# Kernel tuning notes

Measured on AMD Instinct MI355X. Metric: run time of the kernel, lower is better.

## Reference

```python
import jax, jax.numpy as jnp
import numpy as np

D_MODEL = 1024
D_HIDDEN = 4096
NUM_EXPERTS = 8
K_ACTIVE = 2


def setup_inputs() -> dict:
    key = jax.random.key(0)
    ks = jax.random.split(key, 8)
    x = jax.random.normal(ks[0], (1, 2048, D_MODEL), dtype=jnp.float32)
    gate_w = jax.random.normal(ks[1], (D_MODEL, NUM_EXPERTS), dtype=jnp.float32) * 0.02
    gate_b = jnp.zeros((NUM_EXPERTS,), dtype=jnp.float32)
    w1 = jax.random.normal(ks[2], (NUM_EXPERTS, D_MODEL, D_HIDDEN), dtype=jnp.float32) * 0.02
    b1 = jnp.zeros((NUM_EXPERTS, D_HIDDEN), dtype=jnp.float32)
    w2 = jax.random.normal(ks[3], (NUM_EXPERTS, D_HIDDEN, D_MODEL), dtype=jnp.float32) * 0.02
    b2 = jnp.zeros((NUM_EXPERTS, D_MODEL), dtype=jnp.float32)
    return {"x": x, "gate_w": gate_w, "gate_b": gate_b,
            "w1": w1, "b1": b1, "w2": w2, "b2": b2}


def reference(x, gate_w, gate_b, w1, b1, w2, b2):
    B, S, D = x.shape
    xf = x.reshape(-1, D)                                    # [T, D]
    logits = xf @ gate_w + gate_b                            # [T, E]
    top_w, top_idx = jax.lax.top_k(logits, K_ACTIVE)         # [T, K]
    top_w = jax.nn.softmax(top_w, axis=-1)                   # softmax over selected experts
    # combine-weight per expert: sum over k slots of one-hot(idx) * weight -> [T, E]
    gates = jnp.sum(jax.nn.one_hot(top_idx, NUM_EXPERTS, dtype=xf.dtype) * top_w[..., None], axis=1)
    # expert FFN applied per expert (dropout is identity in eval): gelu is exact (erf), matching torch nn.GELU default
    h = jax.nn.gelu(jnp.einsum('td,edh->teh', xf, w1) + b1[None], approximate=False)  # [T, E, H]
    y = jnp.einsum('teh,ehd->ted', h, w2) + b2[None]         # [T, E, D]
    out = jnp.einsum('ted,te->td', y, gates)                 # weighted combine of selected experts
    return out.reshape(B, S, D)
```

## Files before the change

kernel.cpp:

```cpp
#include <hip/hip_runtime.h>
#include <stdint.h>

typedef unsigned short u16;
typedef __attribute__((ext_vector_type(8))) short s16x8;
typedef __attribute__((ext_vector_type(8))) u16  u16x8;
typedef __attribute__((ext_vector_type(4))) u16  u16x4;
typedef __attribute__((ext_vector_type(4))) float f32x4;

#define T_TOKENS 2048
#define DM 1024
#define DH 4096
#define NE 8
#define BM 128
#define BN 128
#define BN2 64
#define BK 64
#define MAXSLOTS (T_TOKENS*2 + NE*BM)
#define ROWBLK (MAXSLOTS/BM)

__device__ __forceinline__ u16 f2bf(float f) {
    union { float ff; uint32_t u; } v; v.ff = f;
    uint32_t r = v.u + 0x7fffu + ((v.u >> 16) & 1u);
    return (u16)(r >> 16);
}

#define GLOAD_LDS16(gsrc, ldst) \
    __builtin_amdgcn_global_load_lds((const __attribute__((address_space(1))) uint32_t*)(gsrc), \
                                     (__attribute__((address_space(3))) uint32_t*)(ldst), 16, 0, 0)

__global__ void k_convert(const float* __restrict__ x, u16* __restrict__ xbf,
                          int* __restrict__ ctrl) {
    int i = blockIdx.x * blockDim.x + threadIdx.x;
    const f32x4* xv = (const f32x4*)x;
    f32x4 a = xv[2*i], b = xv[2*i+1];
    u16x8 o;
    o[0]=f2bf(a[0]); o[1]=f2bf(a[1]); o[2]=f2bf(a[2]); o[3]=f2bf(a[3]);
    o[4]=f2bf(b[0]); o[5]=f2bf(b[1]); o[6]=f2bf(b[2]); o[7]=f2bf(b[3]);
    ((u16x8*)xbf)[i] = o;
    if (blockIdx.x == 0 && threadIdx.x < 32) ctrl[threadIdx.x] = 0;
}

__global__ void __launch_bounds__(256) k_transpose(const float* __restrict__ src,
                                                   u16* __restrict__ dst,
                                                   int K, int N) {
    __shared__ float tile[64][65];
    const int e = blockIdx.z;
    const int n0 = blockIdx.x * 64, k0 = blockIdx.y * 64;
    const float* s = src + (size_t)e * K * N;
    u16* d = dst + (size_t)e * K * N;
    const int tx = threadIdx.x & 15, ty = threadIdx.x >> 4;
    #pragma unroll
    for (int j = 0; j < 4; ++j) {
        int r = ty * 4 + j;
        f32x4 v = *(const f32x4*)(s + (size_t)(k0 + r) * N + n0 + tx * 4);
        tile[r][tx*4+0] = v[0]; tile[r][tx*4+1] = v[1];
        tile[r][tx*4+2] = v[2]; tile[r][tx*4+3] = v[3];
    }
    __syncthreads();
    #pragma unroll
    for (int j = 0; j < 4; ++j) {
        int n = ty * 4 + j;
        u16x4 w;
        #pragma unroll
        for (int c = 0; c < 4; ++c) w[c] = f2bf(tile[tx*4+c][n]);
        *(u16x4*)(d + (size_t)(n0 + n) * K + k0 + tx * 4) = w;
    }
}

__global__ void __launch_bounds__(64) k_gate(const float* __restrict__ x,
                                             const float* __restrict__ gw,
                                             const float* __restrict__ gb,
                                             int* __restrict__ cnt,
                                             int* __restrict__ tt_idx,
                                             float* __restrict__ tt_w) {
    const int t = blockIdx.x;
    const int lane = threadIdx.x;
    float acc[NE] = {0.f,0.f,0.f,0.f,0.f,0.f,0.f,0.f};
    const float* xr = x + (size_t)t * DM;
    #pragma unroll
    for (int c = 0; c < DM/64; ++c) {
        float xv = xr[lane + 64*c];
        const float* g = gw + (size_t)(lane + 64*c) * NE;
        #pragma unroll
        for (int e = 0; e < NE; ++e) acc[e] += xv * g[e];
    }
    #pragma unroll
    for (int e = 0; e < NE; ++e) {
        #pragma unroll
        for (int off = 32; off >= 1; off >>= 1)
            acc[e] += __shfl_xor(acc[e], off, 64);
    }
    if (lane == 0) {
        float l[NE];
        #pragma unroll
        for (int e = 0; e < NE; ++e) l[e] = acc[e] + gb[e];
        int i0 = 0;
        #pragma unroll
        for (int e = 1; e < NE; ++e) if (l[e] > l[i0]) i0 = e;
        int i1 = (i0 == 0) ? 1 : 0;
        #pragma unroll
        for (int e = 0; e < NE; ++e) if (e != i0 && l[e] > l[i1]) i1 = e;
        float m  = l[i0];
        float w0 = expf(l[i0] - m), w1 = expf(l[i1] - m);
        float s = w0 + w1; w0 /= s; w1 /= s;
        tt_idx[t*2] = i0; tt_idx[t*2+1] = i1;
        tt_w[t*2] = w0;  tt_w[t*2+1] = w1;
        atomicAdd(&cnt[i0], 1); atomicAdd(&cnt[i1], 1);
    }
}

__global__ void k_offsets(const int* __restrict__ cnt, int* __restrict__ fill,
                          int* __restrict__ off) {
    if (threadIdx.x == 0 && blockIdx.x == 0) {
        int a = 0;
        for (int e = 0; e < NE; ++e) {
            off[e] = a;
            a += (cnt[e] + BM - 1) / BM * BM;
            fill[e] = 0;
        }
        off[NE] = a;
    }
}

__global__ void k_scatter(const int* __restrict__ tt_idx, const float* __restrict__ tt_w,
                          const int* __restrict__ off, int* __restrict__ fill,
                          int* __restrict__ slot_token, float* __restrict__ slot_gate) {
    int t = blockIdx.x * blockDim.x + threadIdx.x;
    if (t >= T_TOKENS) return;
    #pragma unroll
    for (int k = 0; k < 2; ++k) {
        int e = tt_idx[t*2+k];
        int pos = off[e] + atomicAdd(&fill[e], 1);
        slot_token[pos] = t;
        slot_gate[pos]  = tt_w[t*2+k];
    }
}

__device__ __forceinline__ void mma64(const u16* As, const u16* Bs, int lane,
                                      int wr, int wc, f32x4 acc[4][4]) {
    #pragma unroll
    for (int ko = 0; ko < 2; ++ko) {
        s16x8 af[4], bfr[4];
        #pragma unroll
        for (int m = 0; m < 4; ++m) {
            int row = wr*64 + m*16 + (lane & 15);
            int sl = (ko*4 + (lane >> 4)) ^ (row & 7);
            af[m] = *(const s16x8*)&As[row*BK + sl*8];
        }
        #pragma unroll
        for (int n = 0; n < 4; ++n) {
            int col = wc*64 + n*16 + (lane & 15);
            int sl = (ko*4 + (lane >> 4)) ^ (col & 7);
            bfr[n] = *(const s16x8*)&Bs[col*BK + sl*8];
        }
        #pragma unroll
        for (int m = 0; m < 4; ++m)
            #pragma unroll
            for (int n = 0; n < 4; ++n)
                acc[m][n] = __builtin_amdgcn_mfma_f32_16x16x32_bf16(af[m], bfr[n], acc[m][n], 0, 0, 0);
    }
}

__device__ __forceinline__ void mma64_n2(const u16* As, const u16* Bs, int lane,
                                         int wr, int wc, f32x4 acc[4][2]) {
    #pragma unroll
    for (int ko = 0; ko < 2; ++ko) {
        s16x8 af[4], bfr[2];
        #pragma unroll
        for (int m = 0; m < 4; ++m) {
            int row = wr*64 + m*16 + (lane & 15);
            int sl = (ko*4 + (lane >> 4)) ^ (row & 7);
            af[m] = *(const s16x8*)&As[row*BK + sl*8];
        }
        #pragma unroll
        for (int n = 0; n < 2; ++n) {
            int col = wc*32 + n*16 + (lane & 15);
            int sl = (ko*4 + (lane >> 4)) ^ (col & 7);
            bfr[n] = *(const s16x8*)&Bs[col*BK + sl*8];
        }
        #pragma unroll
        for (int m = 0; m < 4; ++m)
            #pragma unroll
            for (int n = 0; n < 2; ++n)
                acc[m][n] = __builtin_amdgcn_mfma_f32_16x16x32_bf16(af[m], bfr[n], acc[m][n], 0, 0, 0);
    }
}


__global__ void __launch_bounds__(256) k_ffn1_b16(
    const u16* __restrict__ xbf, const u16* __restrict__ w1t,
    const float* __restrict__ b1, const int* __restrict__ slot_token,
    const int* __restrict__ off, u16* __restrict__ h)
{
    __shared__ u16 As[2][BM*BK];
    __shared__ u16 Bs[2][BN*BK];
    const int rb = blockIdx.y, cb = blockIdx.x;
    const int total = off[NE];
    const int r0 = rb * BM;
    if (r0 >= total) return;
    int e = 0;
    while (e < NE-1 && off[e+1] <= r0) e++;
    const u16* Bsrc = w1t + (size_t)e * DM * DH;
    const float* be = b1 + (size_t)e * DH;

    const int tid = threadIdx.x;
    const int lane = tid & 63, wid = tid >> 6;
    const int wr = wid >> 1, wc = wid & 1;

    const u16* gA[4]; const u16* gB[4];
    #pragma unroll
    for (int i = 0; i < 4; ++i) {
        int row = wid*32 + i*8 + (lane >> 3);
        int g = (lane & 7) ^ (row & 7);
        int tok = slot_token[r0 + row];
        gA[i] = xbf + (size_t)tok * DM + g*8;
        gB[i] = Bsrc + (size_t)(cb*BN + row) * DM + g*8;
    }

    f32x4 acc[4][4];
    #pragma unroll
    for (int m = 0; m < 4; ++m)
        #pragma unroll
        for (int n = 0; n < 4; ++n) acc[m][n] = (f32x4){0.f,0.f,0.f,0.f};

    #define STAGE1(buf, kt) do {                                              \
        _Pragma("unroll")                                                     \
        for (int i = 0; i < 4; ++i) {                                         \
            GLOAD_LDS16(gA[i] + (kt)*BK, &As[buf][(wid*32 + i*8)*BK]);        \
            GLOAD_LDS16(gB[i] + (kt)*BK, &Bs[buf][(wid*32 + i*8)*BK]);        \
        }                                                                     \
    } while (0)

    const int NT = DM / BK;
    STAGE1(0, 0);
    __syncthreads();
    #pragma unroll 1
    for (int kt = 0; kt < NT; kt += 2) {
        STAGE1(1, kt + 1);
        mma64(As[0], Bs[0], lane, wr, wc, acc);
        __syncthreads();
        if (kt + 2 < NT) STAGE1(0, kt + 2);
        mma64(As[1], Bs[1], lane, wr, wc, acc);
        __syncthreads();
    }
    #undef STAGE1

    #pragma unroll
    for (int n = 0; n < 4; ++n) {
        int col = cb*BN + wc*64 + n*16 + (lane & 15);
        float bb = be[col];
        #pragma unroll
        for (int m = 0; m < 4; ++m) {
            int rbase = r0 + wr*64 + m*16 + (lane >> 4)*4;
            #pragma unroll
            for (int i = 0; i < 4; ++i) {
                float v = acc[m][n][i] + bb;
                float gv = 0.5f * v * (1.0f + erff(v * 0.70710678118654752f));
                h[(size_t)(rbase + i)*DH + col] = f2bf(gv);
            }
        }
    }
}

__global__ void __launch_bounds__(256) k_ffn2_b16(
    const u16* __restrict__ h, const u16* __restrict__ w2t,
    const float* __restrict__ b2, const int* __restrict__ slot_token,
    const float* __restrict__ slot_gate, const int* __restrict__ off,
    float* __restrict__ out)
{
    __shared__ u16 As[2][BM*BK];
    __shared__ u16 Bs[2][BN2*BK];
    const int rb = blockIdx.y, cb = blockIdx.x;
    const int total = off[NE];
    const int r0 = rb * BM;
    if (r0 >= total) return;
    int e = 0;
    while (e < NE-1 && off[e+1] <= r0) e++;
    const u16* Bsrc = w2t + (size_t)e * DH * DM;
    const float* be = b2 + (size_t)e * DM;

    const int tid = threadIdx.x;
    const int lane = tid & 63, wid = tid >> 6;
    const int wr = wid >> 1, wc = wid & 1;

    const u16* gA[4]; const u16* gB[2];
    #pragma unroll
    for (int i = 0; i < 4; ++i) {
        int row = wid*32 + i*8 + (lane >> 3);
        int g = (lane & 7) ^ (row & 7);
        gA[i] = h + (size_t)(r0 + row) * DH + g*8;
    }
    #pragma unroll
    for (int i = 0; i < 2; ++i) {
        int n = wid*16 + i*8 + (lane >> 3);
        int g = (lane & 7) ^ (n & 7);
        gB[i] = Bsrc + (size_t)(cb*BN2 + n) * DH + g*8;
    }

    f32x4 acc[4][2];
    #pragma unroll
    for (int m = 0; m < 4; ++m)
        #pragma unroll
        for (int n = 0; n < 2; ++n) acc[m][n] = (f32x4){0.f,0.f,0.f,0.f};

    #define STAGE2(buf, kt) do {                                              \
        _Pragma("unroll")                                                     \
        for (int i = 0; i < 4; ++i)                                           \
            GLOAD_LDS16(gA[i] + (kt)*BK, &As[buf][(wid*32 + i*8)*BK]);        \
        _Pragma("unroll")                                                     \
        for (int i = 0; i < 2; ++i)                                           \
            GLOAD_LDS16(gB[i] + (kt)*BK, &Bs[buf][(wid*16 + i*8)*BK]);        \
    } while (0)

    const int NT = DH / BK;
    STAGE2(0, 0);
    __syncthreads();
    #pragma unroll 1
    for (int kt = 0; kt < NT; kt += 2) {
        STAGE2(1, kt + 1);
        mma64_n2(As[0], Bs[0], lane, wr, wc, acc);
        __syncthreads();
        if (kt + 2 < NT) STAGE2(0, kt + 2);
        mma64_n2(As[1], Bs[1], lane, wr, wc, acc);
        __syncthreads();
    }
    #undef STAGE2

    float bb[2];
    #pragma unroll
    for (int n = 0; n < 2; ++n) bb[n] = be[cb*BN2 + wc*32 + n*16 + (lane & 15)];
    #pragma unroll
    for (int m = 0; m < 4; ++m) {
        #pragma unroll
        for (int i = 0; i < 4; ++i) {
            int s = r0 + wr*64 + m*16 + (lane >> 4)*4 + i;
            int tok = slot_token[s];
            float g = slot_gate[s];
            if (g != 0.0f) {
                float* orow = out + (size_t)tok * DM + cb*BN2 + wc*32;
                #pragma unroll
                for (int n = 0; n < 2; ++n)
                    atomicAdd(orow + n*16 + (lane & 15), g * (acc[m][n][i] + bb[n]));
            }
        }
    }
}


__global__ void __launch_bounds__(256) k_ffn1_f32(
    const u16* __restrict__ xbf, const float* __restrict__ w1,
    const float* __restrict__ b1, const int* __restrict__ slot_token,
    const int* __restrict__ off, u16* __restrict__ h)
{
    __shared__ u16 As[BM*BK];
    __shared__ u16 Bs[BN*BK];
    const int rb = blockIdx.y, cb = blockIdx.x;
    const int total = off[NE];
    const int r0 = rb * BM;
    if (r0 >= total) return;
    int e = 0;
    while (e < NE-1 && off[e+1] <= r0) e++;
    const float* Bsrc = w1 + (size_t)e * DM * DH;
    const float* be   = b1 + (size_t)e * DH;

    const int tid = threadIdx.x;
    const int lane = tid & 63, wid = tid >> 6;
    const int wr = wid >> 1, wc = wid & 1;

    const u16* gA[4];
    #pragma unroll
    for (int i = 0; i < 4; ++i) {
        int row = wid*32 + i*8 + (lane >> 3);
        int g = (lane & 7) ^ (row & 7);
        int tok = slot_token[r0 + row];
        gA[i] = xbf + (size_t)tok * DM + g*8;
    }
    const int tc = tid & 31, tr = tid >> 5;
    const float* gB = Bsrc + (size_t)(tr*8) * DH + cb*BN + tc*4;

    f32x4 acc[4][4];
    #pragma unroll
    for (int m = 0; m < 4; ++m)
        #pragma unroll
        for (int n = 0; n < 4; ++n) acc[m][n] = (f32x4){0.f,0.f,0.f,0.f};

    for (int kt = 0; kt < DM/BK; ++kt) {
        #pragma unroll
        for (int i = 0; i < 4; ++i)
            GLOAD_LDS16(gA[i] + kt*BK, &As[(wid*32 + i*8)*BK]);
        f32x4 bv[8];
        #pragma unroll
        for (int j = 0; j < 8; ++j)
            bv[j] = *(const f32x4*)(gB + (size_t)(kt*BK + j) * DH);
        #pragma unroll
        for (int c = 0; c < 4; ++c) {
            int n = tc*4 + c;
            int sl = tr ^ (n & 7);
            s16x8 pk;
            #pragma unroll
            for (int j = 0; j < 8; ++j) pk[j] = (short)f2bf(bv[j][c]);
            *(s16x8*)&Bs[n*BK + sl*8] = pk;
        }
        __syncthreads();
        mma64(As, Bs, lane, wr, wc, acc);
        __syncthreads();
    }
    #pragma unroll
    for (int n = 0; n < 4; ++n) {
        int col = cb*BN + wc*64 + n*16 + (lane & 15);
        float bb = be[col];
        #pragma unroll
        for (int m = 0; m < 4; ++m) {
            int rbase = r0 + wr*64 + m*16 + (lane >> 4)*4;
            #pragma unroll
            for (int i = 0; i < 4; ++i) {
                float v = acc[m][n][i] + bb;
                float gv = 0.5f * v * (1.0f + erff(v * 0.70710678118654752f));
                h[(size_t)(rbase + i)*DH + col] = f2bf(gv);
            }
        }
    }
}

__global__ void __launch_bounds__(256) k_ffn2_f32(
    const u16* __restrict__ h, const float* __restrict__ w2,
    const float* __restrict__ b2, const int* __restrict__ slot_token,
    const float* __restrict__ slot_gate, const int* __restrict__ off,
    float* __restrict__ out)
{
    __shared__ u16 As[BM*BK];
    __shared__ u16 Bs[BN*BK];
    const int rb = blockIdx.y, cb = blockIdx.x;
    const int total = off[NE];
    const int r0 = rb * BM;
    if (r0 >= total) return;
    int e = 0;
    while (e < NE-1 && off[e+1] <= r0) e++;
    const float* Bsrc = w2 + (size_t)e * DH * DM;
    const float* be   = b2 + (size_t)e * DM;

    const int tid = threadIdx.x;
    const int lane = tid & 63, wid = tid >> 6;
    const int wr = wid >> 1, wc = wid & 1;

    const u16* gA[4];
    #pragma unroll
    for (int i = 0; i < 4; ++i) {
        int row = wid*32 + i*8 + (lane >> 3);
        int g = (lane & 7) ^ (row & 7);
        gA[i] = h + (size_t)(r0 + row) * DH + g*8;
    }
    const int tc = tid & 31, tr = tid >> 5;
    const float* gB = Bsrc + (size_t)(tr*8) * DM + cb*BN + tc*4;

    f32x4 acc[4][4];
    #pragma unroll
    for (int m = 0; m < 4; ++m)
        #pragma unroll
        for (int n = 0; n < 4; ++n) acc[m][n] = (f32x4){0.f,0.f,0.f,0.f};

    for (int kt = 0; kt < DH/BK; ++kt) {
        #pragma unroll
        for (int i = 0; i < 4; ++i)
            GLOAD_LDS16(gA[i] + kt*BK, &As[(wid*32 + i*8)*BK]);
        f32x4 bv[8];
        #pragma unroll
        for (int j = 0; j < 8; ++j)
            bv[j] = *(const f32x4*)(gB + (size_t)(kt*BK + j) * DM);
        #pragma unroll
        for (int c = 0; c < 4; ++c) {
            int n = tc*4 + c;
            int sl = tr ^ (n & 7);
            s16x8 pk;
            #pragma unroll
            for (int j = 0; j < 8; ++j) pk[j] = (short)f2bf(bv[j][c]);
            *(s16x8*)&Bs[n*BK + sl*8] = pk;
        }
        __syncthreads();
        mma64(As, Bs, lane, wr, wc, acc);
        __syncthreads();
    }
    float bb[4];
    #pragma unroll
    for (int n = 0; n < 4; ++n) bb[n] = be[cb*BN + wc*64 + n*16 + (lane & 15)];
    #pragma unroll
    for (int m = 0; m < 4; ++m) {
        #pragma unroll
        for (int i = 0; i < 4; ++i) {
            int s = r0 + wr*64 + m*16 + (lane >> 4)*4 + i;
            int tok = slot_token[s];
            float g = slot_gate[s];
            if (g != 0.0f) {
                float* orow = out + (size_t)tok * DM + cb*BN + wc*64;
                #pragma unroll
                for (int n = 0; n < 4; ++n)
                    atomicAdd(orow + n*16 + (lane & 15), g * (acc[m][n][i] + bb[n]));
            }
        }
    }
}

extern "C" void kernel_launch(void* const* d_in, const int* in_sizes, int n_in,
                              void* d_out, int out_size, void* d_ws, size_t ws_size,
                              hipStream_t stream)
{
    (void)in_sizes; (void)n_in; (void)out_size;
    const float* x  = (const float*)d_in[0];
    const float* gw = (const float*)d_in[1];
    const float* gb = (const float*)d_in[2];
    const float* w1 = (const float*)d_in[3];
    const float* b1 = (const float*)d_in[4];
    const float* w2 = (const float*)d_in[5];
    const float* b2 = (const float*)d_in[6];
    float* out = (float*)d_out;
    char* ws = (char*)d_ws;

    const size_t OFF_XBF = 0;
    const size_t OFF_H   = 4194304;
    const size_t OFF_WT  = OFF_H + (size_t)MAXSLOTS * DH * 2;
    const size_t OFF_ST  = OFF_WT + (size_t)NE * DM * DH * 2;
    const size_t OFF_SG  = OFF_ST + MAXSLOTS * 4;
    const size_t OFF_TI  = OFF_SG + MAXSLOTS * 4;
    const size_t OFF_TW  = OFF_TI + T_TOKENS * 2 * 4;
    const size_t OFF_CT  = OFF_TW + T_TOKENS * 2 * 4;
    const size_t NEED_B16 = OFF_CT + 128;

    if (ws_size >= NEED_B16) {
        u16*   xbf        = (u16*)(ws + OFF_XBF);
        u16*   h          = (u16*)(ws + OFF_H);
        u16*   wt         = (u16*)(ws + OFF_WT);
        int*   slot_token = (int*)(ws + OFF_ST);
        float* slot_gate  = (float*)(ws + OFF_SG);
        int*   tt_idx     = (int*)(ws + OFF_TI);
        float* tt_w       = (float*)(ws + OFF_TW);
        int*   ctrl       = (int*)(ws + OFF_CT);
        int* cnt = ctrl; int* fill = ctrl + 8; int* offs = ctrl + 16;

        hipMemsetAsync(slot_token, 0, 2 * MAXSLOTS * 4, stream);
        hipMemsetAsync(out, 0, (size_t)T_TOKENS * DM * sizeof(float), stream);

        k_convert<<<(T_TOKENS*DM/8 + 255)/256, 256, 0, stream>>>(x, xbf, ctrl);
        k_gate<<<T_TOKENS, 64, 0, stream>>>(x, gw, gb, cnt, tt_idx, tt_w);
        k_offsets<<<1, 64, 0, stream>>>(cnt, fill, offs);
        k_scatter<<<(T_TOKENS + 255)/256, 256, 0, stream>>>(tt_idx, tt_w, offs, fill, slot_token, slot_gate);

        k_transpose<<<dim3(DH/64, DM/64, NE), 256, 0, stream>>>(w1, wt, DM, DH);
        k_ffn1_b16<<<dim3(DH/BN, ROWBLK), 256, 0, stream>>>(xbf, wt, b1, slot_token, offs, h);
        k_transpose<<<dim3(DM/64, DH/64, NE), 256, 0, stream>>>(w2, wt, DH, DM);
        k_ffn2_b16<<<dim3(DM/BN2, ROWBLK), 256, 0, stream>>>(h, wt, b2, slot_token, slot_gate, offs, out);
    } else {
        u16*   xbf        = (u16*)(ws);
        u16*   h          = (u16*)(ws + 4194304);
        int*   slot_token = (int*)(ws + 46137344);
        float* slot_gate  = (float*)(ws + 46157824);
        int*   tt_idx     = (int*)(ws + 46178304);
        float* tt_w       = (float*)(ws + 46194688);
        int*   ctrl       = (int*)(ws + 46211072);
        int* cnt = ctrl; int* fill = ctrl + 8; int* offs = ctrl + 16;

        hipMemsetAsync(slot_token, 0, 2 * MAXSLOTS * 4, stream);
        hipMemsetAsync(out, 0, (size_t)T_TOKENS * DM * sizeof(float), stream);

        k_convert<<<(T_TOKENS*DM/8 + 255)/256, 256, 0, stream>>>(x, xbf, ctrl);
        k_gate<<<T_TOKENS, 64, 0, stream>>>(x, gw, gb, cnt, tt_idx, tt_w);
        k_offsets<<<1, 64, 0, stream>>>(cnt, fill, offs);
        k_scatter<<<(T_TOKENS + 255)/256, 256, 0, stream>>>(tt_idx, tt_w, offs, fill, slot_token, slot_gate);
        k_ffn1_f32<<<dim3(DH/BN, ROWBLK), 256, 0, stream>>>(xbf, w1, b1, slot_token, offs, h);
        k_ffn2_f32<<<dim3(DM/BN, ROWBLK), 256, 0, stream>>>(h, w2, b2, slot_token, slot_gate, offs, out);
    }
}
```

Baseline: 322.9 us.

## Triple-buffer FFN GEMM k-loop with vmcnt waits and narrow FFN1 tiles

Both expert GEMM kernels switch from a double-buffered loop with two __syncthreads per step to a three-stage LDS ring. Each step waits only on its own stage with s_waitcnt vmcnt(6), then issues a single barrier, prefetches two tiles ahead, and raises wave priority around the MFMA block. FFN1 also narrows its N tile from 128 to 64 and reuses the 4x2 MFMA helper, which doubles its grid. The aim is to hide global-to-LDS latency and raise occupancy or wave count, at the cost of more LDS per block and more redundant A-tile loads in FFN1.

```diff
diff --git a/kernel.cpp b/kernel.cpp
--- a/kernel.cpp
+++ b/kernel.cpp
@@ -12,8 +12,8 @@
 #define DH 4096
 #define NE 8
 #define BM 128
+#define BNW 64
 #define BN 128
-#define BN2 64
 #define BK 64
 #define MAXSLOTS (T_TOKENS*2 + NE*BM)
 #define ROWBLK (MAXSLOTS/BM)
@@ -27,6 +27,9 @@
 #define GLOAD_LDS16(gsrc, ldst) \
     __builtin_amdgcn_global_load_lds((const __attribute__((address_space(1))) uint32_t*)(gsrc), \
                                      (__attribute__((address_space(3))) uint32_t*)(ldst), 16, 0, 0)
+
+#define WAIT_VM6() asm volatile("s_waitcnt vmcnt(6)" ::: "memory")
+#define WAIT_VM0() asm volatile("s_waitcnt vmcnt(0)" ::: "memory")
 
 __global__ void k_convert(const float* __restrict__ x, u16* __restrict__ xbf,
                           int* __restrict__ ctrl) {
@@ -136,11 +139,11 @@
     }
 }
 
-__device__ __forceinline__ void mma64(const u16* As, const u16* Bs, int lane,
-                                      int wr, int wc, f32x4 acc[4][4]) {
+__device__ __forceinline__ void mma64_n2(const u16* As, const u16* Bs, int lane,
+                                         int wr, int wc, f32x4 acc[4][2]) {
     #pragma unroll
     for (int ko = 0; ko < 2; ++ko) {
-        s16x8 af[4], bfr[4];
+        s16x8 af[4], bfr[2];
         #pragma unroll
         for (int m = 0; m < 4; ++m) {
             int row = wr*64 + m*16 + (lane & 15);
@@ -148,6 +151,31 @@
             af[m] = *(const s16x8*)&As[row*BK + sl*8];
         }
         #pragma unroll
+        for (int n = 0; n < 2; ++n) {
+            int col = wc*32 + n*16 + (lane & 15);
+            int sl = (ko*4 + (lane >> 4)) ^ (col & 7);
+            bfr[n] = *(const s16x8*)&Bs[col*BK + sl*8];
+        }
+        #pragma unroll
+        for (int m = 0; m < 4; ++m)
+            #pragma unroll
+            for (int n = 0; n < 2; ++n)
+                acc[m][n] = __builtin_amdgcn_mfma_f32_16x16x32_bf16(af[m], bfr[n], acc[m][n], 0, 0, 0);
+    }
+}
+
+__device__ __forceinline__ void mma64(const u16* As, const u16* Bs, int lane,
+                                      int wr, int wc, f32x4 acc[4][4]) {
+    #pragma unroll
+    for (int ko = 0; ko < 2; ++ko) {
+        s16x8 af[4], bfr[4];
+        #pragma unroll
+        for (int m = 0; m < 4; ++m) {
+            int row = wr*64 + m*16 + (lane & 15);
+            int sl = (ko*4 + (lane >> 4)) ^ (row & 7);
+            af[m] = *(const s16x8*)&As[row*BK + sl*8];
+        }
+        #pragma unroll
         for (int n = 0; n < 4; ++n) {
             int col = wc*64 + n*16 + (lane & 15);
             int sl = (ko*4 + (lane >> 4)) ^ (col & 7);
@@ -157,31 +185,6 @@
         for (int m = 0; m < 4; ++m)
             #pragma unroll
             for (int n = 0; n < 4; ++n)
-                acc[m][n] = __builtin_amdgcn_mfma_f32_16x16x32_bf16(af[m], bfr[n], acc[m][n], 0, 0, 0);
-    }
-}
-
-__device__ __forceinline__ void mma64_n2(const u16* As, const u16* Bs, int lane,
-                                         int wr, int wc, f32x4 acc[4][2]) {
-    #pragma unroll
-    for (int ko = 0; ko < 2; ++ko) {
-        s16x8 af[4], bfr[2];
-        #pragma unroll
-        for (int m = 0; m < 4; ++m) {
-            int row = wr*64 + m*16 + (lane & 15);
-            int sl = (ko*4 + (lane >> 4)) ^ (row & 7);
-            af[m] = *(const s16x8*)&As[row*BK + sl*8];
-        }
-        #pragma unroll
-        for (int n = 0; n < 2; ++n) {
-            int col = wc*32 + n*16 + (lane & 15);
-            int sl = (ko*4 + (lane >> 4)) ^ (col & 7);
-            bfr[n] = *(const s16x8*)&Bs[col*BK + sl*8];
-        }
-        #pragma unroll
-        for (int m = 0; m < 4; ++m)
-            #pragma unroll
-            for (int n = 0; n < 2; ++n)
                 acc[m][n] = __builtin_amdgcn_mfma_f32_16x16x32_bf16(af[m], bfr[n], acc[m][n], 0, 0, 0);
     }
 }
@@ -192,8 +195,8 @@
     const float* __restrict__ b1, const int* __restrict__ slot_token,
     const int* __restrict__ off, u16* __restrict__ h)
 {
-    __shared__ u16 As[2][BM*BK];
-    __shared__ u16 Bs[2][BN*BK];
+    __shared__ u16 As[3][BM*BK];
+    __shared__ u16 Bs[3][BNW*BK];
     const int rb = blockIdx.y, cb = blockIdx.x;
     const int total = off[NE];
     const int r0 = rb * BM;
@@ -207,47 +210,56 @@
     const int lane = tid & 63, wid = tid >> 6;
     const int wr = wid >> 1, wc = wid & 1;
 
-    const u16* gA[4]; const u16* gB[4];
+    const u16* gA[4]; const u16* gB[2];
     #pragma unroll
     for (int i = 0; i < 4; ++i) {
         int row = wid*32 + i*8 + (lane >> 3);
         int g = (lane & 7) ^ (row & 7);
         int tok = slot_token[r0 + row];
         gA[i] = xbf + (size_t)tok * DM + g*8;
-        gB[i] = Bsrc + (size_t)(cb*BN + row) * DM + g*8;
-    }
-
-    f32x4 acc[4][4];
+    }
+    #pragma unroll
+    for (int i = 0; i < 2; ++i) {
+        int n = wid*16 + i*8 + (lane >> 3);
+        int g = (lane & 7) ^ (n & 7);
+        gB[i] = Bsrc + (size_t)(cb*BNW + n) * DM + g*8;
+    }
+
+    f32x4 acc[4][2];
     #pragma unroll
     for (int m = 0; m < 4; ++m)
         #pragma unroll
-        for (int n = 0; n < 4; ++n) acc[m][n] = (f32x4){0.f,0.f,0.f,0.f};
+        for (int n = 0; n < 2; ++n) acc[m][n] = (f32x4){0.f,0.f,0.f,0.f};
 
     #define STAGE1(buf, kt) do {                                              \
         _Pragma("unroll")                                                     \
-        for (int i = 0; i < 4; ++i) {                                         \
+        for (int i = 0; i < 4; ++i)                                           \
             GLOAD_LDS16(gA[i] + (kt)*BK, &As[buf][(wid*32 + i*8)*BK]);        \
-            GLOAD_LDS16(gB[i] + (kt)*BK, &Bs[buf][(wid*32 + i*8)*BK]);        \
-        }                                                                     \
+        _Pragma("unroll")                                                     \
+        for (int i = 0; i < 2; ++i)                                           \
+            GLOAD_LDS16(gB[i] + (kt)*BK, &Bs[buf][(wid*16 + i*8)*BK]);        \
     } while (0)
 
     const int NT = DM / BK;
     STAGE1(0, 0);
-    __syncthreads();
+    STAGE1(1, 1);
+    int cur = 0, stg = 2;
     #pragma unroll 1
-    for (int kt = 0; kt < NT; kt += 2) {
-        STAGE1(1, kt + 1);
-        mma64(As[0], Bs[0], lane, wr, wc, acc);
-        __syncthreads();
-        if (kt + 2 < NT) STAGE1(0, kt + 2);
-        mma64(As[1], Bs[1], lane, wr, wc, acc);
-        __syncthreads();
+    for (int kt = 0; kt < NT; ++kt) {
+        if (kt < NT - 1) WAIT_VM6(); else WAIT_VM0();
+        __builtin_amdgcn_s_barrier();
+        if (kt + 2 < NT) STAGE1(stg, kt + 2);
+        __builtin_amdgcn_s_setprio(1);
+        mma64_n2(As[cur], Bs[cur], lane, wr, wc, acc);
+        __builtin_amdgcn_s_setprio(0);
+        cur = (cur == 2) ? 0 : cur + 1;
+        stg = (stg == 2) ? 0 : stg + 1;
     }
     #undef STAGE1
 
     #pragma unroll
-    for (int n = 0; n < 4; ++n) {
-        int col = cb*BN + wc*64 + n*16 + (lane & 15);
+    for (int n = 0; n < 2; ++n) {
+        int col = cb*BNW + wc*32 + n*16 + (lane & 15);
         float bb = be[col];
         #pragma unroll
         for (int m = 0; m < 4; ++m) {
@@ -268,8 +280,8 @@
     const float* __restrict__ slot_gate, const int* __restrict__ off,
     float* __restrict__ out)
 {
-    __shared__ u16 As[2][BM*BK];
-    __shared__ u16 Bs[2][BN2*BK];
+    __shared__ u16 As[3][BM*BK];
+    __shared__ u16 Bs[3][BNW*BK];
     const int rb = blockIdx.y, cb = blockIdx.x;
     const int total = off[NE];
     const int r0 = rb * BM;
@@ -294,7 +306,7 @@
     for (int i = 0; i < 2; ++i) {
         int n = wid*16 + i*8 + (lane >> 3);
         int g = (lane & 7) ^ (n & 7);
-        gB[i] = Bsrc + (size_t)(cb*BN2 + n) * DH + g*8;
+        gB[i] = Bsrc + (size_t)(cb*BNW + n) * DH + g*8;
     }
 
     f32x4 acc[4][2];
@@ -314,21 +326,24 @@
 
     const int NT = DH / BK;
     STAGE2(0, 0);
-    __syncthreads();
+    STAGE2(1, 1);
+    int cur = 0, stg = 2;
     #pragma unroll 1
-    for (int kt = 0; kt < NT; kt += 2) {
-        STAGE2(1, kt + 1);
-        mma64_n2(As[0], Bs[0], lane, wr, wc, acc);
-        __syncthreads();
-        if (kt + 2 < NT) STAGE2(0, kt + 2);
-        mma64_n2(As[1], Bs[1], lane, wr, wc, acc);
-        __syncthreads();
+    for (int kt = 0; kt < NT; ++kt) {
+        if (kt < NT - 1) WAIT_VM6(); else WAIT_VM0();
+        __builtin_amdgcn_s_barrier();
+        if (kt + 2 < NT) STAGE2(stg, kt + 2);
+        __builtin_amdgcn_s_setprio(1);
+        mma64_n2(As[cur], Bs[cur], lane, wr, wc, acc);
+        __builtin_amdgcn_s_setprio(0);
+        cur = (cur == 2) ? 0 : cur + 1;
+        stg = (stg == 2) ? 0 : stg + 1;
     }
     #undef STAGE2
 
     float bb[2];
     #pragma unroll
-    for (int n = 0; n < 2; ++n) bb[n] = be[cb*BN2 + wc*32 + n*16 + (lane & 15)];
+    for (int n = 0; n < 2; ++n) bb[n] = be[cb*BNW + wc*32 + n*16 + (lane & 15)];
     #pragma unroll
     for (int m = 0; m < 4; ++m) {
         #pragma unroll
@@ -337,7 +352,7 @@
             int tok = slot_token[s];
             float g = slot_gate[s];
             if (g != 0.0f) {
-                float* orow = out + (size_t)tok * DM + cb*BN2 + wc*32;
+                float* orow = out + (size_t)tok * DM + cb*BNW + wc*32;
                 #pragma unroll
                 for (int n = 0; n < 2; ++n)
                     atomicAdd(orow + n*16 + (lane & 15), g * (acc[m][n][i] + bb[n]));
@@ -545,9 +560,9 @@
         k_scatter<<<(T_TOKENS + 255)/256, 256, 0, stream>>>(tt_idx, tt_w, offs, fill, slot_token, slot_gate);
 
         k_transpose<<<dim3(DH/64, DM/64, NE), 256, 0, stream>>>(w1, wt, DM, DH);
-        k_ffn1_b16<<<dim3(DH/BN, ROWBLK), 256, 0, stream>>>(xbf, wt, b1, slot_token, offs, h);
+        k_ffn1_b16<<<dim3(DH/BNW, ROWBLK), 256, 0, stream>>>(xbf, wt, b1, slot_token, offs, h);
         k_transpose<<<dim3(DM/64, DH/64, NE), 256, 0, stream>>>(w2, wt, DH, DM);
-        k_ffn2_b16<<<dim3(DM/BN2, ROWBLK), 256, 0, stream>>>(h, wt, b2, slot_token, slot_gate, offs, out);
+        k_ffn2_b16<<<dim3(DM/BNW, ROWBLK), 256, 0, stream>>>(h, wt, b2, slot_token, slot_gate, offs, out);
     } else {
         u16*   xbf        = (u16*)(ws);
         u16*   h          = (u16*)(ws + 4194304);
```

New measurement: 368.6 us. +14.2%, slower.

## Pipeline GEMM loads with vmcnt waits and split-K FFN2 with combine kernel

Applied to the files above, without the earlier changes.

Both expert GEMMs now prefetch two stages ahead and wait on the vector-memory counter instead of a full __syncthreads, raising wave priority during MFMA work. FFN2 switches to 128-wide tiles and a split-K of two along the hidden dimension. Each split atomically accumulates into a per-slot partial buffer, and a new combine kernel applies bias and gate weights per token, replacing scattered atomics into the output. This adds a large partial buffer with its memset and an extra launch. The tighter waits rely on the vmcnt accounting being exact.

```diff
diff --git a/kernel.cpp b/kernel.cpp
--- a/kernel.cpp
+++ b/kernel.cpp
@@ -13,7 +13,6 @@
 #define NE 8
 #define BM 128
 #define BN 128
-#define BN2 64
 #define BK 64
 #define MAXSLOTS (T_TOKENS*2 + NE*BM)
 #define ROWBLK (MAXSLOTS/BM)
@@ -27,6 +26,9 @@
 #define GLOAD_LDS16(gsrc, ldst) \
     __builtin_amdgcn_global_load_lds((const __attribute__((address_space(1))) uint32_t*)(gsrc), \
                                      (__attribute__((address_space(3))) uint32_t*)(ldst), 16, 0, 0)
+
+#define WAIT_VM8() asm volatile("s_waitcnt vmcnt(8)" ::: "memory")
+#define WAIT_VM0() asm volatile("s_waitcnt vmcnt(0)" ::: "memory")
 
 __global__ void k_convert(const float* __restrict__ x, u16* __restrict__ xbf,
                           int* __restrict__ ctrl) {
@@ -124,7 +126,8 @@
 
 __global__ void k_scatter(const int* __restrict__ tt_idx, const float* __restrict__ tt_w,
                           const int* __restrict__ off, int* __restrict__ fill,
-                          int* __restrict__ slot_token, float* __restrict__ slot_gate) {
+                          int* __restrict__ slot_token, float* __restrict__ slot_gate,
+                          int* __restrict__ tok_slot) {
     int t = blockIdx.x * blockDim.x + threadIdx.x;
     if (t >= T_TOKENS) return;
     #pragma unroll
@@ -133,6 +136,7 @@
         int pos = off[e] + atomicAdd(&fill[e], 1);
         slot_token[pos] = t;
         slot_gate[pos]  = tt_w[t*2+k];
+        tok_slot[t*2+k] = pos;
     }
 }
 
@@ -157,31 +161,6 @@
         for (int m = 0; m < 4; ++m)
             #pragma unroll
             for (int n = 0; n < 4; ++n)
-                acc[m][n] = __builtin_amdgcn_mfma_f32_16x16x32_bf16(af[m], bfr[n], acc[m][n], 0, 0, 0);
-    }
-}
-
-__device__ __forceinline__ void mma64_n2(const u16* As, const u16* Bs, int lane,
-                                         int wr, int wc, f32x4 acc[4][2]) {
-    #pragma unroll
-    for (int ko = 0; ko < 2; ++ko) {
-        s16x8 af[4], bfr[2];
-        #pragma unroll
-        for (int m = 0; m < 4; ++m) {
-            int row = wr*64 + m*16 + (lane & 15);
-            int sl = (ko*4 + (lane >> 4)) ^ (row & 7);
-            af[m] = *(const s16x8*)&As[row*BK + sl*8];
-        }
-        #pragma unroll
-        for (int n = 0; n < 2; ++n) {
-            int col = wc*32 + n*16 + (lane & 15);
-            int sl = (ko*4 + (lane >> 4)) ^ (col & 7);
-            bfr[n] = *(const s16x8*)&Bs[col*BK + sl*8];
-        }
-        #pragma unroll
-        for (int m = 0; m < 4; ++m)
-            #pragma unroll
-            for (int n = 0; n < 2; ++n)
                 acc[m][n] = __builtin_amdgcn_mfma_f32_16x16x32_bf16(af[m], bfr[n], acc[m][n], 0, 0, 0);
     }
 }
@@ -233,15 +212,16 @@
 
     const int NT = DM / BK;
     STAGE1(0, 0);
-    __syncthreads();
+    STAGE1(1, 1);
     #pragma unroll 1
-    for (int kt = 0; kt < NT; kt += 2) {
-        STAGE1(1, kt + 1);
-        mma64(As[0], Bs[0], lane, wr, wc, acc);
-        __syncthreads();
-        if (kt + 2 < NT) STAGE1(0, kt + 2);
-        mma64(As[1], Bs[1], lane, wr, wc, acc);
-        __syncthreads();
+    for (int kt = 0; kt < NT; ++kt) {
+        if (kt + 1 < NT) WAIT_VM8(); else WAIT_VM0();
+        __builtin_amdgcn_s_barrier();
+        __builtin_amdgcn_s_setprio(1);
+        mma64(As[kt & 1], Bs[kt & 1], lane, wr, wc, acc);
+        __builtin_amdgcn_s_setprio(0);
+        __builtin_amdgcn_s_barrier();
+        if (kt + 2 < NT) STAGE1(kt & 1, kt + 2);
     }
     #undef STAGE1
 
@@ -266,11 +246,11 @@
     const u16* __restrict__ h, const u16* __restrict__ w2t,
     const float* __restrict__ b2, const int* __restrict__ slot_token,
     const float* __restrict__ slot_gate, const int* __restrict__ off,
-    float* __restrict__ out)
+    float* __restrict__ out, float* __restrict__ partial, int ktiles)
 {
     __shared__ u16 As[2][BM*BK];
-    __shared__ u16 Bs[2][BN2*BK];
-    const int rb = blockIdx.y, cb = blockIdx.x;
+    __shared__ u16 Bs[2][BN*BK];
+    const int rb = blockIdx.y, cb = blockIdx.x, kz = blockIdx.z;
     const int total = off[NE];
     const int r0 = rb * BM;
     if (r0 >= total) return;
@@ -278,72 +258,102 @@
     while (e < NE-1 && off[e+1] <= r0) e++;
     const u16* Bsrc = w2t + (size_t)e * DH * DM;
     const float* be = b2 + (size_t)e * DM;
+    const int kt0 = kz * ktiles;
 
     const int tid = threadIdx.x;
     const int lane = tid & 63, wid = tid >> 6;
     const int wr = wid >> 1, wc = wid & 1;
 
-    const u16* gA[4]; const u16* gB[2];
+    const u16* gA[4]; const u16* gB[4];
     #pragma unroll
     for (int i = 0; i < 4; ++i) {
         int row = wid*32 + i*8 + (lane >> 3);
         int g = (lane & 7) ^ (row & 7);
-        gA[i] = h + (size_t)(r0 + row) * DH + g*8;
-    }
-    #pragma unroll
-    for (int i = 0; i < 2; ++i) {
-        int n = wid*16 + i*8 + (lane >> 3);
-        int g = (lane & 7) ^ (n & 7);
-        gB[i] = Bsrc + (size_t)(cb*BN2 + n) * DH + g*8;
-    }
-
-    f32x4 acc[4][2];
+        gA[i] = h + (size_t)(r0 + row) * DH + (size_t)kt0*BK + g*8;
+        gB[i] = Bsrc + (size_t)(cb*BN + row) * DH + (size_t)kt0*BK + g*8;
+    }
+
+    f32x4 acc[4][4];
     #pragma unroll
     for (int m = 0; m < 4; ++m)
         #pragma unroll
-        for (int n = 0; n < 2; ++n) acc[m][n] = (f32x4){0.f,0.f,0.f,0.f};
+        for (int n = 0; n < 4; ++n) acc[m][n] = (f32x4){0.f,0.f,0.f,0.f};
 
     #define STAGE2(buf, kt) do {                                              \
         _Pragma("unroll")                                                     \
-        for (int i = 0; i < 4; ++i)                                           \
+        for (int i = 0; i < 4; ++i) {                                         \
             GLOAD_LDS16(gA[i] + (kt)*BK, &As[buf][(wid*32 + i*8)*BK]);        \
-        _Pragma("unroll")                                                     \
-        for (int i = 0; i < 2; ++i)                                           \
-            GLOAD_LDS16(gB[i] + (kt)*BK, &Bs[buf][(wid*16 + i*8)*BK]);        \
+            GLOAD_LDS16(gB[i] + (kt)*BK, &Bs[buf][(wid*32 + i*8)*BK]);        \
+        }                                                                     \
     } while (0)
 
-    const int NT = DH / BK;
+    const int NT = ktiles;
     STAGE2(0, 0);
-    __syncthreads();
+    STAGE2(1, 1);
     #pragma unroll 1
-    for (int kt = 0; kt < NT; kt += 2) {
-        STAGE2(1, kt + 1);
-        mma64_n2(As[0], Bs[0], lane, wr, wc, acc);
-        __syncthreads();
-        if (kt + 2 < NT) STAGE2(0, kt + 2);
-        mma64_n2(As[1], Bs[1], lane, wr, wc, acc);
-        __syncthreads();
+    for (int kt = 0; kt < NT; ++kt) {
+        if (kt + 1 < NT) WAIT_VM8(); else WAIT_VM0();
+        __builtin_amdgcn_s_barrier();
+        __builtin_amdgcn_s_setprio(1);
+        mma64(As[kt & 1], Bs[kt & 1], lane, wr, wc, acc);
+        __builtin_amdgcn_s_setprio(0);
+        __builtin_amdgcn_s_barrier();
+        if (kt + 2 < NT) STAGE2(kt & 1, kt + 2);
     }
     #undef STAGE2
 
-    float bb[2];
-    #pragma unroll
-    for (int n = 0; n < 2; ++n) bb[n] = be[cb*BN2 + wc*32 + n*16 + (lane & 15)];
-    #pragma unroll
-    for (int m = 0; m < 4; ++m) {
-        #pragma unroll
-        for (int i = 0; i < 4; ++i) {
-            int s = r0 + wr*64 + m*16 + (lane >> 4)*4 + i;
-            int tok = slot_token[s];
-            float g = slot_gate[s];
-            if (g != 0.0f) {
-                float* orow = out + (size_t)tok * DM + cb*BN2 + wc*32;
+    if (partial) {
+        #pragma unroll
+        for (int m = 0; m < 4; ++m) {
+            #pragma unroll
+            for (int i = 0; i < 4; ++i) {
+                int s = r0 + wr*64 + m*16 + (lane >> 4)*4 + i;
+                float* prow = partial + (size_t)s * DM + cb*BN + wc*64;
                 #pragma unroll
-                for (int n = 0; n < 2; ++n)
-                    atomicAdd(orow + n*16 + (lane & 15), g * (acc[m][n][i] + bb[n]));
+                for (int n = 0; n < 4; ++n)
+                    atomicAdd(prow + n*16 + (lane & 15), acc[m][n][i]);
             }
         }
-    }
+    } else {
+        float bb[4];
+        #pragma unroll
+        for (int n = 0; n < 4; ++n) bb[n] = be[cb*BN + wc*64 + n*16 + (lane & 15)];
+        #pragma unroll
+        for (int m = 0; m < 4; ++m) {
+            #pragma unroll
+            for (int i = 0; i < 4; ++i) {
+                int s = r0 + wr*64 + m*16 + (lane >> 4)*4 + i;
+                int tok = slot_token[s];
+                float g = slot_gate[s];
+                if (g != 0.0f) {
+                    float* orow = out + (size_t)tok * DM + cb*BN + wc*64;
+                    #pragma unroll
+                    for (int n = 0; n < 4; ++n)
+                        atomicAdd(orow + n*16 + (lane & 15), g * (acc[m][n][i] + bb[n]));
+                }
+            }
+        }
+    }
+}
+
+__global__ void __launch_bounds__(256) k_combine(
+    const float* __restrict__ partial, const float* __restrict__ b2,
+    const int* __restrict__ tok_slot, const int* __restrict__ tt_idx,
+    const float* __restrict__ tt_w, float* __restrict__ out)
+{
+    const int t = blockIdx.x;
+    const int d = threadIdx.x * 4;
+    const int s0 = tok_slot[t*2], s1 = tok_slot[t*2+1];
+    const int e0 = tt_idx[t*2],  e1 = tt_idx[t*2+1];
+    const float g0 = tt_w[t*2],  g1 = tt_w[t*2+1];
+    f32x4 p0 = *(const f32x4*)(partial + (size_t)s0 * DM + d);
+    f32x4 p1 = *(const f32x4*)(partial + (size_t)s1 * DM + d);
+    f32x4 bb0 = *(const f32x4*)(b2 + (size_t)e0 * DM + d);
+    f32x4 bb1 = *(const f32x4*)(b2 + (size_t)e1 * DM + d);
+    f32x4 o;
+    #pragma unroll
+    for (int c = 0; c < 4; ++c) o[c] = g0 * (p0[c] + bb0[c]) + g1 * (p1[c] + bb1[c]);
+    *(f32x4*)(out + (size_t)t * DM + d) = o;
 }
 
 
@@ -522,8 +532,11 @@
     const size_t OFF_SG  = OFF_ST + MAXSLOTS * 4;
     const size_t OFF_TI  = OFF_SG + MAXSLOTS * 4;
     const size_t OFF_TW  = OFF_TI + T_TOKENS * 2 * 4;
-    const size_t OFF_CT  = OFF_TW + T_TOKENS * 2 * 4;
+    const size_t OFF_TS  = OFF_TW + T_TOKENS * 2 * 4;
+    const size_t OFF_CT  = OFF_TS + T_TOKENS * 2 * 4;
     const size_t NEED_B16 = OFF_CT + 128;
+    const size_t OFF_PT  = (NEED_B16 + 255) & ~(size_t)255;
+    const size_t NEED_SPLIT = OFF_PT + (size_t)MAXSLOTS * DM * 4;
 
     if (ws_size >= NEED_B16) {
         u16*   xbf        = (u16*)(ws + OFF_XBF);
@@ -533,21 +546,36 @@
         float* slot_gate  = (float*)(ws + OFF_SG);
         int*   tt_idx     = (int*)(ws + OFF_TI);
         float* tt_w       = (float*)(ws + OFF_TW);
+        int*   tok_slot   = (int*)(ws + OFF_TS);
         int*   ctrl       = (int*)(ws + OFF_CT);
+        float* partial    = (float*)(ws + OFF_PT);
         int* cnt = ctrl; int* fill = ctrl + 8; int* offs = ctrl + 16;
+        const int use_split = (ws_size >= NEED_SPLIT);
 
         hipMemsetAsync(slot_token, 0, 2 * MAXSLOTS * 4, stream);
-        hipMemsetAsync(out, 0, (size_t)T_TOKENS * DM * sizeof(float), stream);
+        if (use_split)
+            hipMemsetAsync(partial, 0, (size_t)MAXSLOTS * DM * 4, stream);
+        else
+            hipMemsetAsync(out, 0, (size_t)T_TOKENS * DM * sizeof(float), stream);
 
         k_convert<<<(T_TOKENS*DM/8 + 255)/256, 256, 0, stream>>>(x, xbf, ctrl);
         k_gate<<<T_TOKENS, 64, 0, stream>>>(x, gw, gb, cnt, tt_idx, tt_w);
         k_offsets<<<1, 64, 0, stream>>>(cnt, fill, offs);
-        k_scatter<<<(T_TOKENS + 255)/256, 256, 0, stream>>>(tt_idx, tt_w, offs, fill, slot_token, slot_gate);
+        k_scatter<<<(T_TOKENS + 255)/256, 256, 0, stream>>>(tt_idx, tt_w, offs, fill,
+                                                            slot_token, slot_gate, tok_slot);
 
         k_transpose<<<dim3(DH/64, DM/64, NE), 256, 0, stream>>>(w1, wt, DM, DH);
         k_ffn1_b16<<<dim3(DH/BN, ROWBLK), 256, 0, stream>>>(xbf, wt, b1, slot_token, offs, h);
         k_transpose<<<dim3(DM/64, DH/64, NE), 256, 0, stream>>>(w2, wt, DH, DM);
-        k_ffn2_b16<<<dim3(DM/BN2, ROWBLK), 256, 0, stream>>>(h, wt, b2, slot_token, slot_gate, offs, out);
+
+        if (use_split) {
+            k_ffn2_b16<<<dim3(DM/BN, ROWBLK, 2), 256, 0, stream>>>(
+                h, wt, b2, slot_token, slot_gate, offs, out, partial, DH/BK/2);
+            k_combine<<<T_TOKENS, 256, 0, stream>>>(partial, b2, tok_slot, tt_idx, tt_w, out);
+        } else {
+            k_ffn2_b16<<<dim3(DM/BN, ROWBLK, 1), 256, 0, stream>>>(
+                h, wt, b2, slot_token, slot_gate, offs, out, (float*)nullptr, DH/BK);
+        }
     } else {
         u16*   xbf        = (u16*)(ws);
         u16*   h          = (u16*)(ws + 4194304);
@@ -555,7 +583,8 @@
         float* slot_gate  = (float*)(ws + 46157824);
         int*   tt_idx     = (int*)(ws + 46178304);
         float* tt_w       = (float*)(ws + 46194688);
-        int*   ctrl       = (int*)(ws + 46211072);
+        int*   tok_slot   = (int*)(ws + 46211072);
+        int*   ctrl       = (int*)(ws + 46227456);
         int* cnt = ctrl; int* fill = ctrl + 8; int* offs = ctrl + 16;
 
         hipMemsetAsync(slot_token, 0, 2 * MAXSLOTS * 4, stream);
@@ -564,7 +593,8 @@
         k_convert<<<(T_TOKENS*DM/8 + 255)/256, 256, 0, stream>>>(x, xbf, ctrl);
         k_gate<<<T_TOKENS, 64, 0, stream>>>(x, gw, gb, cnt, tt_idx, tt_w);
         k_offsets<<<1, 64, 0, stream>>>(cnt, fill, offs);
-        k_scatter<<<(T_TOKENS + 255)/256, 256, 0, stream>>>(tt_idx, tt_w, offs, fill, slot_token, slot_gate);
+        k_scatter<<<(T_TOKENS + 255)/256, 256, 0, stream>>>(tt_idx, tt_w, offs, fill,
+                                                            slot_token, slot_gate, tok_slot);
         k_ffn1_f32<<<dim3(DH/BN, ROWBLK), 256, 0, stream>>>(xbf, w1, b1, slot_token, offs, h);
         k_ffn2_f32<<<dim3(DM/BN, ROWBLK), 256, 0, stream>>>(h, w2, b2, slot_token, slot_gate, offs, out);
     }
```

After: 341.3 us. 1.06x slower.
